# Performance work log

Measured on AMD Instinct MI355X. Metric: run time of the kernel, lower is better.

## Reference

```python
import jax, jax.numpy as jnp
import numpy as np

N_NODES = 100000
N_EDGES = 1600000
NFEAT, NHID, NCLASS = 128, 64, 16


def setup_inputs() -> dict:
    key = jax.random.key(0)
    ks = jax.random.split(key, 6)
    x = jax.random.normal(ks[0], (N_NODES, NFEAT), dtype=jnp.float32)
    src = jax.random.randint(ks[1], (N_EDGES,), 0, N_NODES)
    dst = jax.random.randint(ks[2], (N_EDGES,), 0, N_NODES)
    # Glorot-ish init for the two GraphConv weights, zero bias (DGL default)
    W1 = jax.random.normal(ks[3], (NFEAT, NHID), dtype=jnp.float32) * (1.0 / np.sqrt(NFEAT))
    b1 = jnp.zeros((NHID,), dtype=jnp.float32)
    W2 = jax.random.normal(ks[4], (NHID, NCLASS), dtype=jnp.float32) * (1.0 / np.sqrt(NHID))
    b2 = jnp.zeros((NCLASS,), dtype=jnp.float32)
    return {"x": x, "src": src, "dst": dst, "W1": W1, "b1": b1, "W2": W2, "b2": b2}


def _graph_conv(h, W, b, src, dst, norm_src, norm_dst, n_nodes):
    """DGL GraphConv with norm='both': D_out^{-1/2} A D_in^{-1/2} h W + b.
    Apply W before aggregation when it reduces dimensionality (DGL's in>out path);
    the math is identical either way."""
    if W.shape[0] > W.shape[1]:
        h = h @ W
    h = h * norm_src[:, None]                                   # scale source feats
    agg = jax.ops.segment_sum(h[src], dst, num_segments=n_nodes)  # sparse A @ h
    agg = agg * norm_dst[:, None]
    if W.shape[0] <= W.shape[1]:
        agg = agg @ W
    return agg + b


def reference(x, src, dst, W1, b1, W2, b2):
    n = x.shape[0]
    ones = jnp.ones(src.shape, dtype=x.dtype)
    out_deg = jax.ops.segment_sum(ones, src, num_segments=n)
    in_deg = jax.ops.segment_sum(ones, dst, num_segments=n)
    norm_src = jnp.maximum(out_deg, 1.0) ** -0.5  # degree clamp as in DGL
    norm_dst = jnp.maximum(in_deg, 1.0) ** -0.5
    h = jax.nn.relu(_graph_conv(x, W1, b1, src, dst, norm_src, norm_dst, n))
    # dropout: p=0 / eval mode -> identity
    h = _graph_conv(h, W2, b2, src, dst, norm_src, norm_dst, n)
    return jax.nn.log_softmax(h, axis=1)
```

## Files before the change

### kernel.cpp

```cpp
#include <hip/hip_runtime.h>
#include <hip/hip_bf16.h>

#define NN 100000
#define NE 1600000
#define NF 128
#define NH 64
#define NC 16
#define NB1 391
#define GBIN 256
#define CHUNK 6250
#define BBUK 196
#define NCB 196
#define NGRP 1563

typedef __attribute__((ext_vector_type(8))) short short8v;
typedef __attribute__((ext_vector_type(4))) float float4v;

__device__ __forceinline__ float us2f(unsigned short u) {
    return __uint_as_float(((unsigned int)u) << 16);
}
__device__ __forceinline__ unsigned short f2us_rn(float f) {
    unsigned int u = __float_as_uint(f);
    return (unsigned short)((u + 0x7FFFu + ((u >> 16) & 1u)) >> 16);
}
__device__ __forceinline__ float ldf(const void* p, size_t i, bool f32) {
    return f32 ? ((const float*)p)[i] : us2f(((const unsigned short*)p)[i]);
}

__global__ void k_sniff(const unsigned short* __restrict__ xu, int* __restrict__ mode) {
    __shared__ int cnt;
    if (threadIdx.x == 0) cnt = 0;
    __syncthreads();
    int c = 0;
    for (int i = threadIdx.x; i < 4096; i += 256) {
        unsigned int e = (xu[i] >> 7) & 0xFFu;
        if (e >= 160u) c++;
    }
    atomicAdd(&cnt, c);
    __syncthreads();
    if (threadIdx.x == 0) mode[0] = (cnt >= 16) ? 1 : 0;
}

__global__ void k_deg(const int4* __restrict__ src4, const int4* __restrict__ dst4,
                      int* __restrict__ deg_out, int* __restrict__ deg_in) {
    int i = blockIdx.x * blockDim.x + threadIdx.x;
    if (i < NE / 4) {
        int4 s = src4[i], d = dst4[i];
        atomicAdd(&deg_out[s.x], 1); atomicAdd(&deg_out[s.y], 1);
        atomicAdd(&deg_out[s.z], 1); atomicAdd(&deg_out[s.w], 1);
        atomicAdd(&deg_in[d.x], 1);  atomicAdd(&deg_in[d.y], 1);
        atomicAdd(&deg_in[d.z], 1);  atomicAdd(&deg_in[d.w], 1);
    }
}

__global__ void k_scatter(const int* __restrict__ src, const int* __restrict__ dst,
                          int* __restrict__ cursor, int* __restrict__ srcs_sorted) {
    int e = blockIdx.x * blockDim.x + threadIdx.x;
    if (e < NE) {
        int p = atomicAdd(&cursor[dst[e]], 1);
        srcs_sorted[p] = src[e];
    }
}

__global__ __launch_bounds__(256) void k_hist2(const int* __restrict__ src,
                                               const int* __restrict__ dst,
                                               int* __restrict__ counts_d,
                                               int* __restrict__ counts_s) {
    __shared__ int hd[BBUK], hs[BBUK];
    for (int i = threadIdx.x; i < BBUK; i += 256) { hd[i] = 0; hs[i] = 0; }
    __syncthreads();
    const int g = blockIdx.x;
    const int e0 = g * CHUNK;
    for (int i = threadIdx.x; i < CHUNK; i += 256) {
        atomicAdd(&hd[dst[e0 + i] >> 9], 1);
        atomicAdd(&hs[src[e0 + i] >> 9], 1);
    }
    __syncthreads();
    for (int i = threadIdx.x; i < BBUK; i += 256) {
        counts_d[i * GBIN + g] = hd[i];
        counts_s[i * GBIN + g] = hs[i];
    }
}

__global__ void k_cs_a(const int* __restrict__ counts, int* __restrict__ csum) {
    __shared__ int s[256];
    int i = blockIdx.x * 256 + threadIdx.x;
    s[threadIdx.x] = counts[i];
    __syncthreads();
    for (int off = 128; off > 0; off >>= 1) {
        if (threadIdx.x < off) s[threadIdx.x] += s[threadIdx.x + off];
        __syncthreads();
    }
    if (threadIdx.x == 0) csum[blockIdx.x] = s[0];
}

__global__ void k_cs_b2(const int* __restrict__ csum, int* __restrict__ coff) {
    __shared__ int s[512];
    int t = threadIdx.x;
    int half = t >> 8, j = t & 255;
    s[t] = (j < NCB) ? csum[half * NCB + j] : 0;
    __syncthreads();
    for (int off = 1; off < 256; off <<= 1) {
        int v = (j >= off) ? s[t - off] : 0;
        __syncthreads();
        s[t] += v;
        __syncthreads();
    }
    if (j < NCB) coff[half * NCB + j] = (j == 0) ? 0 : s[t - 1];
}

__global__ void k_cs_c(int* __restrict__ counts, const int* __restrict__ coff) {
    __shared__ int s[256];
    int t = threadIdx.x;
    int i = blockIdx.x * 256 + t;
    int v = counts[i];
    s[t] = v;
    __syncthreads();
    for (int off = 1; off < 256; off <<= 1) {
        int u = (t >= off) ? s[t - off] : 0;
        __syncthreads();
        s[t] += u;
        __syncthreads();
    }
    counts[i] = s[t] - v + coff[blockIdx.x];
}

__global__ __launch_bounds__(256) void k_binscatter2(const int* __restrict__ src,
                                                     const int* __restrict__ dst,
                                                     const int* __restrict__ counts_d,
                                                     const int* __restrict__ counts_s,
                                                     unsigned int* __restrict__ packed,
                                                     unsigned short* __restrict__ packed2) {
    __shared__ int curd[BBUK], curs[BBUK];
    const int g = blockIdx.x;
    for (int i = threadIdx.x; i < BBUK; i += 256) {
        curd[i] = counts_d[i * GBIN + g];
        curs[i] = counts_s[i * GBIN + g];
    }
    __syncthreads();
    const int e0 = g * CHUNK;
    for (int i = threadIdx.x; i < CHUNK; i += 256) {
        int s = src[e0 + i], d = dst[e0 + i];
        int pd = atomicAdd(&curd[d >> 9], 1);
        packed[pd] = ((unsigned)s << 9) | (unsigned)(d & 511);
        int ps = atomicAdd(&curs[s >> 9], 1);
        packed2[ps] = (unsigned short)(s & 511);
    }
}

__global__ __launch_bounds__(256) void k_bdeg_in(const int* __restrict__ counts_d,
                                                 const unsigned int* __restrict__ packed,
                                                 int* __restrict__ deg_in) {
    __shared__ int h[512];
    const int b = blockIdx.x;
    const int n0 = b << 9;
    const int nlim = (NN - n0 < 512) ? (NN - n0) : 512;
    for (int j = threadIdx.x; j < 512; j += 256) h[j] = 0;
    __syncthreads();
    const int beg = counts_d[b * GBIN];
    const int end = (b + 1 < BBUK) ? counts_d[(b + 1) * GBIN] : NE;
    for (int i = beg + threadIdx.x; i < end; i += 256)
        atomicAdd(&h[packed[i] & 511u], 1);
    __syncthreads();
    for (int j = threadIdx.x; j < nlim; j += 256) deg_in[n0 + j] = h[j];
}

__global__ __launch_bounds__(256) void k_bdeg_out(const int* __restrict__ counts_s,
                                                  const unsigned short* __restrict__ packed2,
                                                  int* __restrict__ deg_out) {
    __shared__ int h[512];
    const int b = blockIdx.x;
    const int n0 = b << 9;
    const int nlim = (NN - n0 < 512) ? (NN - n0) : 512;
    for (int j = threadIdx.x; j < 512; j += 256) h[j] = 0;
    __syncthreads();
    const int beg = counts_s[b * GBIN];
    const int end = (b + 1 < BBUK) ? counts_s[(b + 1) * GBIN] : NE;
    for (int i = beg + threadIdx.x; i < end; i += 256)
        atomicAdd(&h[packed2[i] & 511u], 1);
    __syncthreads();
    for (int j = threadIdx.x; j < nlim; j += 256) deg_out[n0 + j] = h[j];
}

__global__ void k_scan_a(const int* __restrict__ deg_in, int* __restrict__ bsum) {
    __shared__ int s[256];
    int i = blockIdx.x * 256 + threadIdx.x;
    s[threadIdx.x] = (i < NN) ? deg_in[i] : 0;
    __syncthreads();
    for (int off = 128; off > 0; off >>= 1) {
        if (threadIdx.x < off) s[threadIdx.x] += s[threadIdx.x + off];
        __syncthreads();
    }
    if (threadIdx.x == 0) bsum[blockIdx.x] = s[0];
}

__global__ void k_scan_b(const int* __restrict__ bsum, int* __restrict__ boff) {
    __shared__ int s[512];
    int t = threadIdx.x;
    s[t] = (t < NB1) ? bsum[t] : 0;
    __syncthreads();
    for (int off = 1; off < 512; off <<= 1) {
        int v = (t >= off) ? s[t - off] : 0;
        __syncthreads();
        s[t] += v;
        __syncthreads();
    }
    if (t < NB1) boff[t] = (t == 0) ? 0 : s[t - 1];
}

__global__ void k_scan_c(const int* __restrict__ deg_in, const int* __restrict__ deg_out,
                         const int* __restrict__ boff, int* __restrict__ row_off,
                         int* __restrict__ cursor, float* __restrict__ nsrc,
                         float* __restrict__ ndst) {
    __shared__ int s[256];
    int t = threadIdx.x;
    int i = blockIdx.x * 256 + t;
    int d = (i < NN) ? deg_in[i] : 0;
    s[t] = d;
    __syncthreads();
    for (int off = 1; off < 256; off <<= 1) {
        int v = (t >= off) ? s[t - off] : 0;
        __syncthreads();
        s[t] += v;
        __syncthreads();
    }
    int excl = s[t] - d + boff[blockIdx.x];
    if (i < NN) {
        row_off[i] = excl;
        cursor[i]  = excl;
        ndst[i] = rsqrtf(fmaxf((float)d, 1.0f));
        nsrc[i] = rsqrtf(fmaxf((float)deg_out[i], 1.0f));
        if (i == NN - 1) row_off[NN] = excl + d;
    }
}

__global__ __launch_bounds__(256) void k_bucketC512(const int* __restrict__ row_off,
                                                    const unsigned int* __restrict__ packed,
                                                    int* __restrict__ srcs_sorted) {
    __shared__ int lcur[512];
    const int n0 = blockIdx.x << 9;
    const int nlim = (NN - n0 < 512) ? (NN - n0) : 512;
    for (int j = threadIdx.x; j < 512; j += 256)
        lcur[j] = (j < nlim) ? row_off[n0 + j] : 0;
    __syncthreads();
    const int beg = row_off[n0];
    const int end = row_off[n0 + nlim];
    for (int i = beg + threadIdx.x; i < end; i += 256) {
        unsigned v = packed[i];
        int p = atomicAdd(&lcur[v & 511u], 1);
        srcs_sorted[p] = (int)(v >> 9);
    }
}

__global__ void k_prepW(const void* __restrict__ W1, unsigned short* __restrict__ W1f,
                        const int* __restrict__ mode) {
    const bool f32 = (mode[0] != 0);
    for (int i = threadIdx.x; i < 1024; i += 256) {
        const int kcnt = i >> 6, lane = i & 63;
        const int kc = kcnt >> 2, nt = kcnt & 3;
        const int quad = lane >> 4, col = lane & 15;
        #pragma unroll
        for (int j = 0; j < 8; ++j) {
            const size_t idx = (size_t)(kc * 32 + quad * 8 + j) * NH + nt * 16 + col;
            W1f[(size_t)i * 8 + j] = f32 ? f2us_rn(((const float*)W1)[idx])
                                         : ((const unsigned short*)W1)[idx];
        }
    }
}

__global__ __launch_bounds__(256) void k_gemm1_mfma(
    const void* __restrict__ x, const unsigned short* __restrict__ W1f,
    const float* __restrict__ nsrc, unsigned short* __restrict__ h1,
    const int* __restrict__ mode)
{
    const bool f32 = (mode[0] != 0);
    const int tid = threadIdx.x;
    const int wave = tid >> 6, lane = tid & 63;
    const int col = lane & 15, quad = lane >> 4;

    short8v bfrag[16];
    #pragma unroll
    for (int f = 0; f < 16; ++f)
        bfrag[f] = *(const short8v*)(W1f + ((size_t)f * 64 + lane) * 8);

    const int base = blockIdx.x * 64 + wave * 16;
    int arow = base + col;
    if (arow > NN - 1) arow = NN - 1;

    short8v afrag[4];
    if (f32) {
        const float4* ap = (const float4*)((const float*)x + (size_t)arow * NF);
        #pragma unroll
        for (int kc = 0; kc < 4; ++kc) {
            float4 v0 = ap[kc * 8 + quad * 2];
            float4 v1 = ap[kc * 8 + quad * 2 + 1];
            short8v af;
            af[0] = (short)f2us_rn(v0.x); af[1] = (short)f2us_rn(v0.y);
            af[2] = (short)f2us_rn(v0.z); af[3] = (short)f2us_rn(v0.w);
            af[4] = (short)f2us_rn(v1.x); af[5] = (short)f2us_rn(v1.y);
            af[6] = (short)f2us_rn(v1.z); af[7] = (short)f2us_rn(v1.w);
            afrag[kc] = af;
        }
    } else {
        const uint4* ap = (const uint4*)((const unsigned short*)x + (size_t)arow * NF);
        #pragma unroll
        for (int kc = 0; kc < 4; ++kc) {
            uint4 v = ap[kc * 4 + quad];
            afrag[kc] = *reinterpret_cast<const short8v*>(&v);
        }
    }

    float4v acc[4];
    #pragma unroll
    for (int nt = 0; nt < 4; ++nt) acc[nt] = (float4v){0.f, 0.f, 0.f, 0.f};
    #pragma unroll
    for (int kc = 0; kc < 4; ++kc)
        #pragma unroll
        for (int nt = 0; nt < 4; ++nt)
            acc[nt] = __builtin_amdgcn_mfma_f32_16x16x32_bf16(afrag[kc], bfrag[kc * 4 + nt], acc[nt], 0, 0, 0);

    #pragma unroll
    for (int reg = 0; reg < 4; ++reg) {
        const int row = base + quad * 4 + reg;
        if (row < NN) {
            const float ns = nsrc[row];
            unsigned short* hp = h1 + (size_t)row * NH + col;
            hp[0]  = f2us_rn(acc[0][reg] * ns);
            hp[16] = f2us_rn(acc[1][reg] * ns);
            hp[32] = f2us_rn(acc[2][reg] * ns);
            hp[48] = f2us_rn(acc[3][reg] * ns);
        }
    }
}

__global__ __launch_bounds__(256) void k_agg1csr(
    const int* __restrict__ row_off, const int* __restrict__ srcs,
    const unsigned short* __restrict__ h1, const float* __restrict__ ndst,
    const float* __restrict__ nsrc, const void* __restrict__ b1,
    const void* __restrict__ W2, const int* __restrict__ mode,
    unsigned short* __restrict__ h2)
{
    const bool f32 = (mode[0] != 0);
    const int lane = threadIdx.x & 63;
    const int q  = lane >> 4;
    const int li = lane & 15;

    const float bias0 = ldf(b1, 4*li+0, f32), bias1 = ldf(b1, 4*li+1, f32);
    const float bias2 = ldf(b1, 4*li+2, f32), bias3 = ldf(b1, 4*li+3, f32);
    float w2[4][4];
    #pragma unroll
    for (int j = 0; j < 4; ++j)
        #pragma unroll
        for (int m = 0; m < 4; ++m)
            w2[j][m] = ldf(W2, (size_t)(4*li+j)*NC + (q + 4*m), f32);

    const int wid = (blockIdx.x * blockDim.x + threadIdx.x) >> 6;
    const int nw  = (gridDim.x * blockDim.x) >> 6;

    for (int row = wid; row < NN; row += nw) {
        const int beg = row_off[row], end = row_off[row + 1];
        float ax = 0.f, ay = 0.f, az = 0.f, aw = 0.f;
        float bx = 0.f, by = 0.f, bz = 0.f, bw = 0.f;
        int i = beg + q;
        int s0 = (i     < end) ? srcs[i]     : 0;
        int s1 = (i + 4 < end) ? srcs[i + 4] : 0;
        while (i + 4 < end) {
            uint2 v0 = *(const uint2*)(h1 + (size_t)s0 * NH + 4*li);
            uint2 v1 = *(const uint2*)(h1 + (size_t)s1 * NH + 4*li);
            const int inext = i + 8;
            s0 = (inext     < end) ? srcs[inext]     : 0;
            s1 = (inext + 4 < end) ? srcs[inext + 4] : 0;
            ax += us2f((unsigned short)(v0.x & 0xFFFF));
            ay += us2f((unsigned short)(v0.x >> 16));
            az += us2f((unsigned short)(v0.y & 0xFFFF));
            aw += us2f((unsigned short)(v0.y >> 16));
            bx += us2f((unsigned short)(v1.x & 0xFFFF));
            by += us2f((unsigned short)(v1.x >> 16));
            bz += us2f((unsigned short)(v1.y & 0xFFFF));
            bw += us2f((unsigned short)(v1.y >> 16));
            i = inext;
        }
        if (i < end) {
            uint2 v0 = *(const uint2*)(h1 + (size_t)s0 * NH + 4*li);
            ax += us2f((unsigned short)(v0.x & 0xFFFF));
            ay += us2f((unsigned short)(v0.x >> 16));
            az += us2f((unsigned short)(v0.y & 0xFFFF));
            aw += us2f((unsigned short)(v0.y >> 16));
        }
        ax += bx; ay += by; az += bz; aw += bw;
        ax += __shfl_xor(ax, 16); ay += __shfl_xor(ay, 16);
        az += __shfl_xor(az, 16); aw += __shfl_xor(aw, 16);
        ax += __shfl_xor(ax, 32); ay += __shfl_xor(ay, 32);
        az += __shfl_xor(az, 32); aw += __shfl_xor(aw, 32);

        const float nd = ndst[row];
        const float t0 = fmaxf(fmaf(ax, nd, bias0), 0.f);
        const float t1 = fmaxf(fmaf(ay, nd, bias1), 0.f);
        const float t2 = fmaxf(fmaf(az, nd, bias2), 0.f);
        const float t3 = fmaxf(fmaf(aw, nd, bias3), 0.f);

        float p0 = fmaf(t0,w2[0][0],fmaf(t1,w2[1][0],fmaf(t2,w2[2][0],t3*w2[3][0])));
        float p1 = fmaf(t0,w2[0][1],fmaf(t1,w2[1][1],fmaf(t2,w2[2][1],t3*w2[3][1])));
        float p2 = fmaf(t0,w2[0][2],fmaf(t1,w2[1][2],fmaf(t2,w2[2][2],t3*w2[3][2])));
        float p3 = fmaf(t0,w2[0][3],fmaf(t1,w2[1][3],fmaf(t2,w2[2][3],t3*w2[3][3])));
        #pragma unroll
        for (int off = 1; off <= 8; off <<= 1) {
            p0 += __shfl_xor(p0, off);
            p1 += __shfl_xor(p1, off);
            p2 += __shfl_xor(p2, off);
            p3 += __shfl_xor(p3, off);
        }
        if (li < 4) {
            float v = (li == 0) ? p0 : (li == 1) ? p1 : (li == 2) ? p2 : p3;
            h2[(size_t)row * NC + q + 4*li] = f2us_rn(v * nsrc[row]);
        }
    }
}

__global__ __launch_bounds__(256) void k_out(
    const int* __restrict__ row_off, const int* __restrict__ srcs,
    const unsigned short* __restrict__ h2, const float* __restrict__ ndst,
    const void* __restrict__ b2, const int* __restrict__ mode,
    void* __restrict__ out)
{
    const bool f32 = (mode[0] != 0);
    const int lane = threadIdx.x & 63;
    const int q  = lane >> 4;
    const int li = lane & 15;
    const float b2v = ldf(b2, li, f32);

    const int wid = (blockIdx.x * blockDim.x + threadIdx.x) >> 6;
    const int nw  = (gridDim.x * blockDim.x) >> 6;

    for (int r = wid; r < NN; r += nw) {
        const int beg = row_off[r], end = row_off[r + 1];
        float a = 0.f, b = 0.f;
        int i = beg + q;
        int s0 = (i     < end) ? srcs[i]     : 0;
        int s1 = (i + 4 < end) ? srcs[i + 4] : 0;
        while (i + 4 < end) {
            float va = us2f(h2[(size_t)s0 * NC + li]);
            float vb = us2f(h2[(size_t)s1 * NC + li]);
            const int inext = i + 8;
            s0 = (inext     < end) ? srcs[inext]     : 0;
            s1 = (inext + 4 < end) ? srcs[inext + 4] : 0;
            a += va; b += vb;
            i = inext;
        }
        if (i < end) a += us2f(h2[(size_t)s0 * NC + li]);
        a += b;
        a += __shfl_xor(a, 16);
        a += __shfl_xor(a, 32);
        float v = fmaf(a, ndst[r], b2v);
        float m = v;
        #pragma unroll
        for (int off = 8; off >= 1; off >>= 1) m = fmaxf(m, __shfl_xor(m, off));
        float ex = __expf(v - m);
        float sm = ex;
        #pragma unroll
        for (int off = 8; off >= 1; off >>= 1) sm += __shfl_xor(sm, off);
        float res = v - m - __logf(sm);
        if (lane < 16) {
            if (f32) ((float*)out)[(size_t)r * NC + li] = res;
            else ((__hip_bfloat16*)out)[(size_t)r * NC + li] = __float2bfloat16(res);
        }
    }
}

extern "C" void kernel_launch(void* const* d_in, const int* in_sizes, int n_in,
                              void* d_out, int out_size, void* d_ws, size_t ws_size,
                              hipStream_t stream) {
    const void* x  = d_in[0];
    const int* src = (const int*)d_in[1];
    const int* dst = (const int*)d_in[2];
    const void* W1 = d_in[3];
    const void* b1 = d_in[4];
    const void* W2 = d_in[5];
    const void* b2 = d_in[6];

    char* ws = (char*)d_ws;
    const size_t O_MODE = 0;
    const size_t O_W1F  = 1024;
    const size_t O_CNT  = O_W1F + 16384;
    const size_t O_CS   = O_CNT  + 401408;
    const size_t O_DEG  = O_CS   + 4096;
    const size_t O_NSRC = O_DEG  + 800000;
    const size_t O_NDST = O_NSRC + 400000;
    const size_t O_ROW  = O_NDST + 400000;
    const size_t O_CUR  = O_ROW  + 400128;
    const size_t O_BS   = O_CUR  + 400128;
    const size_t O_SRCS = O_BS   + 4096;
    const size_t O_H2   = O_SRCS + 6400000;
    const size_t O_H1   = O_H2   + 3200000;
    const size_t NEED = O_H1 + 12800000;
    const bool fast_csr = ws_size >= NEED;

    int*   mode     = (int*)(ws + O_MODE);
    unsigned short* W1f = (unsigned short*)(ws + O_W1F);
    int*   counts_d = (int*)(ws + O_CNT);
    int*   counts_s = counts_d + BBUK * GBIN;
    int*   csum     = (int*)(ws + O_CS);
    int*   coff     = (int*)(ws + O_CS + 2048);
    int*   deg_out  = (int*)(ws + O_DEG);
    int*   deg_in   = deg_out + NN;
    float* nsrc     = (float*)(ws + O_NSRC);
    float* ndst     = (float*)(ws + O_NDST);
    int*   row_off  = (int*)(ws + O_ROW);
    int*   cursor   = (int*)(ws + O_CUR);
    int*   bsum     = (int*)(ws + O_BS);
    int*   boff     = (int*)(ws + O_BS + 2048);
    int*   srcs_s   = (int*)(ws + O_SRCS);
    unsigned short* h2 = (unsigned short*)(ws + O_H2);
    unsigned short* h1 = (unsigned short*)(ws + O_H1);
    unsigned int*   packed  = (unsigned int*)(ws + O_H1);
    unsigned short* packed2 = (unsigned short*)(ws + O_H1 + 6400000);

    k_sniff<<<1, 256, 0, stream>>>((const unsigned short*)x, mode);
    k_prepW<<<1, 256, 0, stream>>>(W1, W1f, mode);
    if (fast_csr) {
        k_hist2<<<GBIN, 256, 0, stream>>>(src, dst, counts_d, counts_s);
        k_cs_a<<<2 * NCB, 256, 0, stream>>>(counts_d, csum);
        k_cs_b2<<<1, 512, 0, stream>>>(csum, coff);
        k_cs_c<<<2 * NCB, 256, 0, stream>>>(counts_d, coff);
        k_binscatter2<<<GBIN, 256, 0, stream>>>(src, dst, counts_d, counts_s, packed, packed2);
        k_bdeg_in<<<BBUK, 256, 0, stream>>>(counts_d, packed, deg_in);
        k_bdeg_out<<<BBUK, 256, 0, stream>>>(counts_s, packed2, deg_out);
        k_scan_a<<<NB1, 256, 0, stream>>>(deg_in, bsum);
        k_scan_b<<<1, 512, 0, stream>>>(bsum, boff);
        k_scan_c<<<NB1, 256, 0, stream>>>(deg_in, deg_out, boff, row_off, cursor, nsrc, ndst);
        k_bucketC512<<<BBUK, 256, 0, stream>>>(row_off, packed, srcs_s);
    } else {
        hipMemsetAsync(deg_out, 0, 2 * (size_t)NN * sizeof(int), stream);
        k_deg<<<(NE / 4 + 255) / 256, 256, 0, stream>>>((const int4*)src, (const int4*)dst, deg_out, deg_in);
        k_scan_a<<<NB1, 256, 0, stream>>>(deg_in, bsum);
        k_scan_b<<<1, 512, 0, stream>>>(bsum, boff);
        k_scan_c<<<NB1, 256, 0, stream>>>(deg_in, deg_out, boff, row_off, cursor, nsrc, ndst);
        k_scatter<<<(NE + 255) / 256, 256, 0, stream>>>(src, dst, cursor, srcs_s);
    }
    k_gemm1_mfma<<<NGRP, 256, 0, stream>>>(x, W1f, nsrc, h1, mode);
    k_agg1csr<<<2048, 256, 0, stream>>>(row_off, srcs_s, h1, ndst, nsrc, b1, W2, mode, h2);
    k_out<<<2048, 256, 0, stream>>>(row_off, srcs_s, h2, ndst, b2, mode, d_out);
}
```

Before: 290.8 us.

## Fuse degree count, CSR scan and bucketing into one per-bucket kernel; vectorize output gather

On the fast CSR path, the separate in-degree histogram, three global scan kernels and the bucket scatter are merged into one per-bucket kernel. It counts degrees in shared memory, does a local Blelloch scan offset by the bucket start, and writes row offsets, ndst and the sorted sources. The out-degree kernel now writes nsrc directly. The final layer's gather reads two bf16 features per lane with 32-bit loads and packs the output stores. This removes four launches and the global deg/scan round trips, at the cost of a longer per-block critical path.

After: 279.0 us. 1.04x faster.

```diff
diff --git a/kernel.cpp b/kernel.cpp
--- a/kernel.cpp
+++ b/kernel.cpp
@@ -62,6 +62,58 @@
     }
 }
 
+__global__ void k_scan_a(const int* __restrict__ deg_in, int* __restrict__ bsum) {
+    __shared__ int s[256];
+    int i = blockIdx.x * 256 + threadIdx.x;
+    s[threadIdx.x] = (i < NN) ? deg_in[i] : 0;
+    __syncthreads();
+    for (int off = 128; off > 0; off >>= 1) {
+        if (threadIdx.x < off) s[threadIdx.x] += s[threadIdx.x + off];
+        __syncthreads();
+    }
+    if (threadIdx.x == 0) bsum[blockIdx.x] = s[0];
+}
+
+__global__ void k_scan_b(const int* __restrict__ bsum, int* __restrict__ boff) {
+    __shared__ int s[512];
+    int t = threadIdx.x;
+    s[t] = (t < NB1) ? bsum[t] : 0;
+    __syncthreads();
+    for (int off = 1; off < 512; off <<= 1) {
+        int v = (t >= off) ? s[t - off] : 0;
+        __syncthreads();
+        s[t] += v;
+        __syncthreads();
+    }
+    if (t < NB1) boff[t] = (t == 0) ? 0 : s[t - 1];
+}
+
+__global__ void k_scan_c(const int* __restrict__ deg_in, const int* __restrict__ deg_out,
+                         const int* __restrict__ boff, int* __restrict__ row_off,
+                         int* __restrict__ cursor, float* __restrict__ nsrc,
+                         float* __restrict__ ndst) {
+    __shared__ int s[256];
+    int t = threadIdx.x;
+    int i = blockIdx.x * 256 + t;
+    int d = (i < NN) ? deg_in[i] : 0;
+    s[t] = d;
+    __syncthreads();
+    for (int off = 1; off < 256; off <<= 1) {
+        int v = (t >= off) ? s[t - off] : 0;
+        __syncthreads();
+        s[t] += v;
+        __syncthreads();
+    }
+    int excl = s[t] - d + boff[blockIdx.x];
+    if (i < NN) {
+        row_off[i] = excl;
+        cursor[i]  = excl;
+        ndst[i] = rsqrtf(fmaxf((float)d, 1.0f));
+        nsrc[i] = rsqrtf(fmaxf((float)deg_out[i], 1.0f));
+        if (i == NN - 1) row_off[NN] = excl + d;
+    }
+}
+
 __global__ __launch_bounds__(256) void k_hist2(const int* __restrict__ src,
                                                const int* __restrict__ dst,
                                                int* __restrict__ counts_d,
@@ -148,106 +200,83 @@
     }
 }
 
-__global__ __launch_bounds__(256) void k_bdeg_in(const int* __restrict__ counts_d,
-                                                 const unsigned int* __restrict__ packed,
-                                                 int* __restrict__ deg_in) {
+__global__ __launch_bounds__(256) void k_bdeg_out_nsrc(const int* __restrict__ counts_s,
+                                                       const unsigned short* __restrict__ packed2,
+                                                       float* __restrict__ nsrc) {
     __shared__ int h[512];
     const int b = blockIdx.x;
     const int n0 = b << 9;
     const int nlim = (NN - n0 < 512) ? (NN - n0) : 512;
     for (int j = threadIdx.x; j < 512; j += 256) h[j] = 0;
     __syncthreads();
-    const int beg = counts_d[b * GBIN];
-    const int end = (b + 1 < BBUK) ? counts_d[(b + 1) * GBIN] : NE;
+    const int beg = counts_s[b * GBIN];
+    const int end = (b + 1 < BBUK) ? counts_s[(b + 1) * GBIN] : NE;
     for (int i = beg + threadIdx.x; i < end; i += 256)
-        atomicAdd(&h[packed[i] & 511u], 1);
-    __syncthreads();
-    for (int j = threadIdx.x; j < nlim; j += 256) deg_in[n0 + j] = h[j];
-}
-
-__global__ __launch_bounds__(256) void k_bdeg_out(const int* __restrict__ counts_s,
-                                                  const unsigned short* __restrict__ packed2,
-                                                  int* __restrict__ deg_out) {
+        atomicAdd(&h[packed2[i] & 511u], 1);
+    __syncthreads();
+    for (int j = threadIdx.x; j < nlim; j += 256)
+        nsrc[n0 + j] = rsqrtf(fmaxf((float)h[j], 1.0f));
+}
+
+__global__ __launch_bounds__(256) void k_bucket_all(const int* __restrict__ counts_d,
+                                                    const unsigned int* __restrict__ packed,
+                                                    int* __restrict__ row_off,
+                                                    float* __restrict__ ndst,
+                                                    int* __restrict__ srcs_sorted) {
     __shared__ int h[512];
     const int b = blockIdx.x;
     const int n0 = b << 9;
     const int nlim = (NN - n0 < 512) ? (NN - n0) : 512;
-    for (int j = threadIdx.x; j < 512; j += 256) h[j] = 0;
-    __syncthreads();
-    const int beg = counts_s[b * GBIN];
-    const int end = (b + 1 < BBUK) ? counts_s[(b + 1) * GBIN] : NE;
-    for (int i = beg + threadIdx.x; i < end; i += 256)
-        atomicAdd(&h[packed2[i] & 511u], 1);
-    __syncthreads();
-    for (int j = threadIdx.x; j < nlim; j += 256) deg_out[n0 + j] = h[j];
-}
-
-__global__ void k_scan_a(const int* __restrict__ deg_in, int* __restrict__ bsum) {
-    __shared__ int s[256];
-    int i = blockIdx.x * 256 + threadIdx.x;
-    s[threadIdx.x] = (i < NN) ? deg_in[i] : 0;
-    __syncthreads();
-    for (int off = 128; off > 0; off >>= 1) {
-        if (threadIdx.x < off) s[threadIdx.x] += s[threadIdx.x + off];
-        __syncthreads();
-    }
-    if (threadIdx.x == 0) bsum[blockIdx.x] = s[0];
-}
-
-__global__ void k_scan_b(const int* __restrict__ bsum, int* __restrict__ boff) {
-    __shared__ int s[512];
-    int t = threadIdx.x;
-    s[t] = (t < NB1) ? bsum[t] : 0;
-    __syncthreads();
-    for (int off = 1; off < 512; off <<= 1) {
-        int v = (t >= off) ? s[t - off] : 0;
-        __syncthreads();
-        s[t] += v;
-        __syncthreads();
-    }
-    if (t < NB1) boff[t] = (t == 0) ? 0 : s[t - 1];
-}
-
-__global__ void k_scan_c(const int* __restrict__ deg_in, const int* __restrict__ deg_out,
-                         const int* __restrict__ boff, int* __restrict__ row_off,
-                         int* __restrict__ cursor, float* __restrict__ nsrc,
-                         float* __restrict__ ndst) {
-    __shared__ int s[256];
-    int t = threadIdx.x;
-    int i = blockIdx.x * 256 + t;
-    int d = (i < NN) ? deg_in[i] : 0;
-    s[t] = d;
-    __syncthreads();
-    for (int off = 1; off < 256; off <<= 1) {
-        int v = (t >= off) ? s[t - off] : 0;
-        __syncthreads();
-        s[t] += v;
-        __syncthreads();
-    }
-    int excl = s[t] - d + boff[blockIdx.x];
-    if (i < NN) {
-        row_off[i] = excl;
-        cursor[i]  = excl;
-        ndst[i] = rsqrtf(fmaxf((float)d, 1.0f));
-        nsrc[i] = rsqrtf(fmaxf((float)deg_out[i], 1.0f));
-        if (i == NN - 1) row_off[NN] = excl + d;
-    }
-}
-
-__global__ __launch_bounds__(256) void k_bucketC512(const int* __restrict__ row_off,
-                                                    const unsigned int* __restrict__ packed,
-                                                    int* __restrict__ srcs_sorted) {
-    __shared__ int lcur[512];
-    const int n0 = blockIdx.x << 9;
-    const int nlim = (NN - n0 < 512) ? (NN - n0) : 512;
-    for (int j = threadIdx.x; j < 512; j += 256)
-        lcur[j] = (j < nlim) ? row_off[n0 + j] : 0;
-    __syncthreads();
-    const int beg = row_off[n0];
-    const int end = row_off[n0 + nlim];
-    for (int i = beg + threadIdx.x; i < end; i += 256) {
+    const int t = threadIdx.x;
+    for (int j = t; j < 512; j += 256) h[j] = 0;
+    __syncthreads();
+    const int beg = counts_d[b * GBIN];
+    const int end = (b + 1 < BBUK) ? counts_d[(b + 1) * GBIN] : NE;
+    for (int i = beg + t; i < end; i += 256)
+        atomicAdd(&h[packed[i] & 511u], 1);
+    __syncthreads();
+    const int degA = h[t], degB = h[t + 256];
+    int offset = 1;
+    #pragma unroll
+    for (int d = 256; d > 0; d >>= 1) {
+        __syncthreads();
+        if (t < d) {
+            int ai = offset * (2 * t + 1) - 1;
+            int bi = offset * (2 * t + 2) - 1;
+            h[bi] += h[ai];
+        }
+        offset <<= 1;
+    }
+    __syncthreads();
+    if (t == 0) h[511] = 0;
+    #pragma unroll
+    for (int d = 1; d < 512; d <<= 1) {
+        offset >>= 1;
+        __syncthreads();
+        if (t < d) {
+            int ai = offset * (2 * t + 1) - 1;
+            int bi = offset * (2 * t + 2) - 1;
+            int tmp = h[ai]; h[ai] = h[bi]; h[bi] += tmp;
+        }
+    }
+    __syncthreads();
+    const int r0 = beg + h[t];
+    const int r1 = beg + h[t + 256];
+    if (t < nlim) {
+        row_off[n0 + t] = r0;
+        ndst[n0 + t] = rsqrtf(fmaxf((float)degA, 1.0f));
+    }
+    if (t + 256 < nlim) {
+        row_off[n0 + t + 256] = r1;
+        ndst[n0 + t + 256] = rsqrtf(fmaxf((float)degB, 1.0f));
+    }
+    if (n0 + nlim == NN && t == 0) row_off[NN] = end;
+    __syncthreads();
+    h[t] = r0; h[t + 256] = r1;
+    __syncthreads();
+    for (int i = beg + t; i < end; i += 256) {
         unsigned v = packed[i];
-        int p = atomicAdd(&lcur[v & 511u], 1);
+        int p = atomicAdd(&h[v & 511u], 1);
         srcs_sorted[p] = (int)(v >> 9);
     }
 }
@@ -425,44 +454,62 @@
 {
     const bool f32 = (mode[0] != 0);
     const int lane = threadIdx.x & 63;
-    const int q  = lane >> 4;
-    const int li = lane & 15;
-    const float b2v = ldf(b2, li, f32);
+    const int q  = lane >> 3;
+    const int li = lane & 7;
+    const float b2v0 = ldf(b2, 2*li,   f32);
+    const float b2v1 = ldf(b2, 2*li+1, f32);
 
     const int wid = (blockIdx.x * blockDim.x + threadIdx.x) >> 6;
     const int nw  = (gridDim.x * blockDim.x) >> 6;
 
     for (int r = wid; r < NN; r += nw) {
         const int beg = row_off[r], end = row_off[r + 1];
-        float a = 0.f, b = 0.f;
+        float a0 = 0.f, a1 = 0.f, c0 = 0.f, c1 = 0.f;
         int i = beg + q;
         int s0 = (i     < end) ? srcs[i]     : 0;
-        int s1 = (i + 4 < end) ? srcs[i + 4] : 0;
-        while (i + 4 < end) {
-            float va = us2f(h2[(size_t)s0 * NC + li]);
-            float vb = us2f(h2[(size_t)s1 * NC + li]);
-            const int inext = i + 8;
+        int s1 = (i + 8 < end) ? srcs[i + 8] : 0;
+        while (i + 8 < end) {
+            unsigned u0 = *(const unsigned*)(h2 + (size_t)s0 * NC + 2*li);
+            unsigned u1 = *(const unsigned*)(h2 + (size_t)s1 * NC + 2*li);
+            const int inext = i + 16;
             s0 = (inext     < end) ? srcs[inext]     : 0;
-            s1 = (inext + 4 < end) ? srcs[inext + 4] : 0;
-            a += va; b += vb;
+            s1 = (inext + 8 < end) ? srcs[inext + 8] : 0;
+            a0 += us2f((unsigned short)(u0 & 0xFFFF));
+            a1 += us2f((unsigned short)(u0 >> 16));
+            c0 += us2f((unsigned short)(u1 & 0xFFFF));
+            c1 += us2f((unsigned short)(u1 >> 16));
             i = inext;
         }
-        if (i < end) a += us2f(h2[(size_t)s0 * NC + li]);
-        a += b;
-        a += __shfl_xor(a, 16);
-        a += __shfl_xor(a, 32);
-        float v = fmaf(a, ndst[r], b2v);
-        float m = v;
-        #pragma unroll
-        for (int off = 8; off >= 1; off >>= 1) m = fmaxf(m, __shfl_xor(m, off));
-        float ex = __expf(v - m);
-        float sm = ex;
-        #pragma unroll
-        for (int off = 8; off >= 1; off >>= 1) sm += __shfl_xor(sm, off);
-        float res = v - m - __logf(sm);
-        if (lane < 16) {
-            if (f32) ((float*)out)[(size_t)r * NC + li] = res;
-            else ((__hip_bfloat16*)out)[(size_t)r * NC + li] = __float2bfloat16(res);
+        if (i < end) {
+            unsigned u0 = *(const unsigned*)(h2 + (size_t)s0 * NC + 2*li);
+            a0 += us2f((unsigned short)(u0 & 0xFFFF));
+            a1 += us2f((unsigned short)(u0 >> 16));
+        }
+        a0 += c0; a1 += c1;
+        #pragma unroll
+        for (int off = 8; off <= 32; off <<= 1) {
+            a0 += __shfl_xor(a0, off);
+            a1 += __shfl_xor(a1, off);
+        }
+        const float nd = ndst[r];
+        float v0 = fmaf(a0, nd, b2v0);
+        float v1 = fmaf(a1, nd, b2v1);
+        float m = fmaxf(v0, v1);
+        #pragma unroll
+        for (int off = 1; off <= 4; off <<= 1) m = fmaxf(m, __shfl_xor(m, off));
+        float sm = __expf(v0 - m) + __expf(v1 - m);
+        #pragma unroll
+        for (int off = 1; off <= 4; off <<= 1) sm += __shfl_xor(sm, off);
+        const float lsm = __logf(sm);
+        const float r0 = v0 - m - lsm, r1 = v1 - m - lsm;
+        if (q == 0) {
+            if (f32) {
+                float2 o; o.x = r0; o.y = r1;
+                *(float2*)((float*)out + (size_t)r * NC + 2*li) = o;
+            } else {
+                unsigned o = ((unsigned)f2us_rn(r1) << 16) | (unsigned)f2us_rn(r0);
+                *(unsigned*)((unsigned short*)out + (size_t)r * NC + 2*li) = o;
+            }
         }
     }
 }
@@ -523,12 +570,8 @@
         k_cs_b2<<<1, 512, 0, stream>>>(csum, coff);
         k_cs_c<<<2 * NCB, 256, 0, stream>>>(counts_d, coff);
         k_binscatter2<<<GBIN, 256, 0, stream>>>(src, dst, counts_d, counts_s, packed, packed2);
-        k_bdeg_in<<<BBUK, 256, 0, stream>>>(counts_d, packed, deg_in);
-        k_bdeg_out<<<BBUK, 256, 0, stream>>>(counts_s, packed2, deg_out);
-        k_scan_a<<<NB1, 256, 0, stream>>>(deg_in, bsum);
-        k_scan_b<<<1, 512, 0, stream>>>(bsum, boff);
-        k_scan_c<<<NB1, 256, 0, stream>>>(deg_in, deg_out, boff, row_off, cursor, nsrc, ndst);
-        k_bucketC512<<<BBUK, 256, 0, stream>>>(row_off, packed, srcs_s);
+        k_bdeg_out_nsrc<<<BBUK, 256, 0, stream>>>(counts_s, packed2, nsrc);
+        k_bucket_all<<<BBUK, 256, 0, stream>>>(counts_d, packed, row_off, ndst, srcs_s);
     } else {
         hipMemsetAsync(deg_out, 0, 2 * (size_t)NN * sizeof(int), stream);
         k_deg<<<(NE / 4 + 255) / 256, 256, 0, stream>>>((const int4*)src, (const int4*)dst, deg_out, deg_in);
```
